# Optimization experiments

Measured on AMD Instinct MI355X. Metric: run time of the kernel, lower is better.

## Reference

```python
import jax, jax.numpy as jnp
import numpy as np

H = 16
D_MODEL = 1024
D_K = D_MODEL // H


def setup_inputs() -> dict:
    key = jax.random.key(0)
    ks = jax.random.split(key, 8)
    B, S = 4, 2048
    query = jax.random.normal(ks[0], (B, S, D_MODEL), dtype=jnp.float32)
    key_t = jax.random.normal(ks[1], (B, S, D_MODEL), dtype=jnp.float32)
    value = jax.random.normal(ks[2], (B, S, D_MODEL), dtype=jnp.float32)
    mask = jax.random.randint(ks[3], (B, S, S), 0, 2, dtype=jnp.int32)
    sc = 1.0 / np.sqrt(D_MODEL)
    Wq = jax.random.normal(ks[4], (D_MODEL, D_MODEL), dtype=jnp.float32) * sc
    Wk = jax.random.normal(ks[5], (D_MODEL, D_MODEL), dtype=jnp.float32) * sc
    Wv = jax.random.normal(ks[6], (D_MODEL, D_MODEL), dtype=jnp.float32) * sc
    Wo = jax.random.normal(ks[7], (D_MODEL, D_MODEL), dtype=jnp.float32) * sc
    return {"query": query, "key": key_t, "value": value, "mask": mask,
            "Wq": Wq, "Wk": Wk, "Wv": Wv, "Wo": Wo}


def reference(query, key, value, mask, Wq, Wk, Wv, Wo):
    B, S, _ = query.shape
    # nn.Linear(bias=False): y = x @ W^T; then split heads -> [B,H,S,d_k]
    def proj(x, W):
        return (x @ W.T).reshape(B, S, H, D_K).transpose(0, 2, 1, 3)

    q = proj(query, Wq)
    k = proj(key, Wk)
    v = proj(value, Wv)

    m = (mask[:, None, :, :] != 0)  # [B,1,S,S] broadcast over heads
    scores = jnp.einsum('bhqd,bhkd->bhqk', q, k) / jnp.sqrt(jnp.float32(D_K))
    scores = jnp.where(m, scores, jnp.float32(-1e9))
    p_attn = jax.nn.softmax(scores, axis=-1)
    p_attn = jnp.where(m, p_attn, 0.0)
    # dropout is identity in eval mode
    x = jnp.einsum('bhqk,bhkd->bhqd', p_attn, v)
    x = x.transpose(0, 2, 1, 3).reshape(B, S, D_MODEL)
    return x @ Wo.T
```

## Files before the change

kernel.cpp:

```cpp
#include <hip/hip_runtime.h>


typedef __attribute__((ext_vector_type(8))) short frag8;
typedef __attribute__((ext_vector_type(4))) float f32x4;
typedef unsigned long long ull;

#define MFMA16(a,b,c) __builtin_amdgcn_mfma_f32_16x16x32_bf16((a),(b),(c),0,0,0)

__device__ __forceinline__ short f2bf(float f) {
  union { float f; unsigned u; } x; x.f = f;
  unsigned r = (x.u + 0x7fffu + ((x.u >> 16) & 1u)) >> 16;
  return (short)r;
}

__device__ __forceinline__ unsigned pkbf(float lo, float hi) {
  union { float f; unsigned u; } a, b;
  a.f = lo; b.f = hi;
  return __builtin_amdgcn_perm(b.u + 0x8000u, a.u + 0x8000u, 0x07060302u);
}

__device__ __forceinline__ unsigned pkbf_t(float lo, float hi) {
  union { float f; unsigned u; } a, b;
  a.f = lo; b.f = hi;
  return __builtin_amdgcn_perm(b.u, a.u, 0x07060302u);
}

__device__ __forceinline__ unsigned bit2m(unsigned word, int off) {
  unsigned r;
  asm("v_bfe_i32 %0, %1, %2, 1" : "=v"(r) : "v"(word), "v"(off));
  return r;
}
__device__ __forceinline__ unsigned mk2(unsigned word, int base) {
  return __builtin_amdgcn_perm(bit2m(word, base + 1), bit2m(word, base),
                               0x05040100u);
}

__device__ __forceinline__ void gl16(const void* g, void* l) {
  __builtin_amdgcn_global_load_lds(
      (const __attribute__((address_space(1))) unsigned*)g,
      (__attribute__((address_space(3))) unsigned*)l, 16, 0, 0);
}

__global__ __launch_bounds__(256) void cast_qkv(
    const float* __restrict__ q, const float* __restrict__ k,
    const float* __restrict__ v, short* __restrict__ qo,
    short* __restrict__ ko, short* __restrict__ vo) {
  int z = blockIdx.x >> 13;
  int i = (blockIdx.x & 8191) * 256 + threadIdx.x;
  const float* s = z == 0 ? q : z == 1 ? k : v;
  short* d = z == 0 ? qo : z == 1 ? ko : vo;
  float4 f = ((const float4*)s)[i];
  short4 o;
  o.x = f2bf(f.x); o.y = f2bf(f.y); o.z = f2bf(f.z); o.w = f2bf(f.w);
  ((short4*)d)[i] = o;
}

__global__ __launch_bounds__(256) void cast_w(
    const float* __restrict__ wq, const float* __restrict__ wk,
    const float* __restrict__ wv, const float* __restrict__ wo,
    short* __restrict__ oq, short* __restrict__ ok,
    short* __restrict__ ov, short* __restrict__ oo) {
  int z = blockIdx.x >> 10;
  int i = (blockIdx.x & 1023) * 256 + threadIdx.x;
  const float* s = z == 0 ? wq : z == 1 ? wk : z == 2 ? wv : wo;
  short* d = z == 0 ? oq : z == 1 ? ok : z == 2 ? ov : oo;
  float sc = (z == 0) ? 0.18033688011f : 1.0f;
  float4 f = ((const float4*)s)[i];
  short4 o;
  o.x = f2bf(f.x * sc); o.y = f2bf(f.y * sc);
  o.z = f2bf(f.z * sc); o.w = f2bf(f.w * sc);
  ((short4*)d)[i] = o;
}

__global__ __launch_bounds__(256) void pack_mask(
    const int* __restrict__ mask, ull* __restrict__ bits) {
  int wv = threadIdx.x >> 6, l = threadIdx.x & 63;
  size_t row = (size_t)blockIdx.x * 4 + wv;
  const int* src = mask + row * 2048;
  for (int c = 0; c < 2048; c += 64) {
    ull bl = __ballot(src[c + l] != 0);
    if (l == 0) bits[(size_t)(c >> 6) * 8192 + row] = bl;
  }
}

template <int MODE>
__device__ __forceinline__ void gemm_body(const short* __restrict__ A,
                                          const short* __restrict__ W,
                                          void* __restrict__ outp, int bid) {
  __shared__ short As[2][128 * 32];
  __shared__ short Bs[2][128 * 32];
  const int t = threadIdx.x;
  const int l = t & 63, wv = t >> 6;
  const int lg = l >> 4, lr = l & 15;
  const int wm = (wv >> 1) * 64, wn = (wv & 1) * 64;
  const int m0 = (bid >> 3) * 128;
  const int n0 = (bid & 7) * 128;

  auto stage = [&](int buf, int kt) {
    const int k0 = kt * 32;
#pragma unroll
    for (int c = 0; c < 2; ++c) {
      int idx = c * 256 + t;
      int row = idx >> 2, ch = (idx & 3) * 8;
      gl16(A + (size_t)(m0 + row) * 1024 + k0 + ch, &As[buf][idx * 8]);
      gl16(W + (size_t)(n0 + row) * 1024 + k0 + ch, &Bs[buf][idx * 8]);
    }
  };

  f32x4 acc[4][4] = {};
  stage(0, 0);
  asm volatile("s_waitcnt vmcnt(0)" ::: "memory");
  __syncthreads();
  int buf = 0;
  for (int kt = 0; kt < 32; ++kt) {
    if (kt + 1 < 32) stage(buf ^ 1, kt + 1);
    frag8 af[4], bf[4];
#pragma unroll
    for (int i = 0; i < 4; ++i) {
      af[i] = *(const frag8*)&As[buf][(wm + i * 16 + lr) * 32 + 8 * lg];
      bf[i] = *(const frag8*)&Bs[buf][(wn + i * 16 + lr) * 32 + 8 * lg];
    }
    __builtin_amdgcn_s_setprio(1);
#pragma unroll
    for (int mi = 0; mi < 4; ++mi)
#pragma unroll
      for (int ni = 0; ni < 4; ++ni)
        acc[mi][ni] = MFMA16(af[mi], bf[ni], acc[mi][ni]);
    __builtin_amdgcn_s_setprio(0);
    asm volatile("s_waitcnt vmcnt(0)" ::: "memory");
    __syncthreads();
    buf ^= 1;
  }

#pragma unroll
  for (int mi = 0; mi < 4; ++mi)
#pragma unroll
    for (int ni = 0; ni < 4; ++ni)
#pragma unroll
      for (int r = 0; r < 4; ++r) {
        int m = m0 + wm + mi * 16 + 4 * lg + r;
        int n = n0 + wn + ni * 16 + lr;
        if (MODE == 0) {
          int b = m >> 11, s = m & 2047, h = n >> 6, dk = n & 63;
          ((short*)outp)[(((size_t)b * 16 + h) * 2048 + s) * 64 + dk] =
              f2bf(acc[mi][ni][r]);
        } else {
          ((float*)outp)[(size_t)m * 1024 + n] = acc[mi][ni][r];
        }
      }
}

__global__ __launch_bounds__(256) void gemm_qkv(
    const short* __restrict__ A0, const short* __restrict__ A1,
    const short* __restrict__ A2, const short* __restrict__ W0,
    const short* __restrict__ W1, const short* __restrict__ W2,
    short* __restrict__ O0, short* __restrict__ O1, short* __restrict__ O2) {
  int wg = (blockIdx.x & 7) * 192 + (blockIdx.x >> 3);
  int z = wg >> 9, bid = wg & 511;
  const short* A = z == 0 ? A0 : z == 1 ? A1 : A2;
  const short* W = z == 0 ? W0 : z == 1 ? W1 : W2;
  short* O = z == 0 ? O0 : z == 1 ? O1 : O2;
  gemm_body<0>(A, W, O, bid);
}

__global__ __launch_bounds__(256) void gemm_o(
    const short* __restrict__ A, const short* __restrict__ W,
    float* __restrict__ O) {
  int bid = (blockIdx.x & 7) * 64 + (blockIdx.x >> 3);
  gemm_body<1>(A, W, O, bid);
}

__global__ __launch_bounds__(256) void transpose_v(
    const short* __restrict__ Vp, short* __restrict__ Vt) {
  __shared__ short lds[64 * 72];
  int bh = blockIdx.y, s0 = blockIdx.x * 64;
  int t = threadIdx.x;
  int rr = t >> 3, c0 = (t & 7) * 8;
#pragma unroll
  for (int half = 0; half < 2; ++half) {
    int r = half * 32 + rr;
    frag8 v = *(const frag8*)(Vp + ((size_t)bh * 2048 + s0 + r) * 64 + c0);
#pragma unroll
    for (int j = 0; j < 8; ++j) lds[r * 72 + c0 + j] = v[j];
  }
  __syncthreads();
#pragma unroll
  for (int half = 0; half < 2; ++half) {
    int d = half * 32 + rr;
    frag8 o;
#pragma unroll
    for (int j = 0; j < 8; ++j) o[j] = lds[(c0 + j) * 72 + d];
    *(frag8*)(Vt + ((size_t)bh * 64 + d) * 2048 + s0 + c0) = o;
  }
}

__global__ __launch_bounds__(256, 4) void attn_fwd(
    const short* __restrict__ Qp, const short* __restrict__ Kp,
    const short* __restrict__ Vt, const ull* __restrict__ mb64,
    short* __restrict__ X) {
  __shared__ short Ks[2][64 * 64];
  __shared__ short Vs[64 * 64];
  __shared__ short Ps[4][16 * 64];

  const int wg = (blockIdx.x & 7) * 128 + (blockIdx.x >> 3);
  const int qt = wg & 15, bh = wg >> 4;
  const int b = bh >> 4, h = bh & 15;
  const int t = threadIdx.x;
  const int l = t & 63, wv = t >> 6;
  const int lg = l >> 4, lr = l & 15;
  const int q0 = qt * 128 + wv * 32;
  const int qrow_base = b << 11;

  frag8 qf[2][2];
  const short* Qb = Qp + ((size_t)bh * 2048 + q0) * 64;
#pragma unroll
  for (int qb = 0; qb < 2; ++qb)
#pragma unroll
    for (int kc = 0; kc < 2; ++kc)
      qf[qb][kc] = *(const frag8*)(Qb + (qb * 16 + lr) * 64 + kc * 32 + 8 * lg);

  f32x4 acc[4][2] = {};
  f32x4 accl[2] = {};

  const size_t kbase = (size_t)bh * 2048 * 64;
  const size_t vbase = (size_t)bh * 64 * 2048;
  short* Pw = &Ps[wv][0];
  const int sx = lr & 7;

  frag8 ones;
#pragma unroll
  for (int j = 0; j < 8; ++j) ones[j] = (short)0x3F80;

  auto stageK = [&](int buf, int kt) {
#pragma unroll
    for (int p = 0; p < 2; ++p) {
      int idx = p * 256 + t;
      int row = idx >> 3, c = idx & 7;
      int cs = (c ^ (row & 7)) * 8;
      gl16(Kp + kbase + (size_t)(kt * 64 + row) * 64 + cs, &Ks[buf][idx * 8]);
    }
  };
  auto stageV = [&](int kt) {
#pragma unroll
    for (int p = 0; p < 2; ++p) {
      int idx = p * 256 + t;
      int row = idx >> 3, c = idx & 7;
      int cs = (c ^ (row & 7)) * 8;
      gl16(Vt + vbase + (size_t)row * 2048 + kt * 64 + cs, &Vs[idx * 8]);
    }
  };

  const uint2* mbp = (const uint2*)mb64;
  const int row0 = qrow_base + q0 + lr;
  const int row1 = row0 + 16;
  uint2 mw0 = mbp[row0], mw1 = mbp[row1];

  stageK(0, 0);
  asm volatile("s_waitcnt vmcnt(0)" ::: "memory");
  __syncthreads();
  int buf = 0;

  for (int kt = 0; kt < 32; ++kt) {
    uint2 mwc0 = mw0, mwc1 = mw1;
    const int nk = (kt + 1) & 31;
    mw0 = mbp[(size_t)nk * 8192 + row0];
    mw1 = mbp[(size_t)nk * 8192 + row1];
    asm volatile("" ::: "memory");
    stageV(kt);
    asm volatile("" ::: "memory");
    stageK(buf ^ 1, nk);

    f32x4 s[4][2] = {};
    __builtin_amdgcn_s_setprio(1);
#pragma unroll
    for (int nb = 0; nb < 4; ++nb) {
      const int ro = (nb * 16 + lr) * 64;
      frag8 k0 = *(const frag8*)&Ks[buf][ro + ((0 + lg) ^ sx) * 8];
      frag8 k1 = *(const frag8*)&Ks[buf][ro + ((4 + lg) ^ sx) * 8];
#pragma unroll
      for (int qb = 0; qb < 2; ++qb) {
        s[nb][qb] = MFMA16(k0, qf[qb][0], s[nb][qb]);
        s[nb][qb] = MFMA16(k1, qf[qb][1], s[nb][qb]);
      }
    }
    __builtin_amdgcn_s_setprio(0);

    auto softmax_store = [&](int qb, uint2 mwq) {
      const int q64 = lr * 64;
#pragma unroll
      for (int nb = 0; nb < 4; ++nb) {
        unsigned word = (nb & 2) ? mwq.y : mwq.x;
        int base = (nb & 1) * 16 + 4 * lg;
        float e0 = __builtin_amdgcn_exp2f(s[nb][qb][0]);
        float e1 = __builtin_amdgcn_exp2f(s[nb][qb][1]);
        float e2 = __builtin_amdgcn_exp2f(s[nb][qb][2]);
        float e3 = __builtin_amdgcn_exp2f(s[nb][qb][3]);
        uint2 w;
        w.x = pkbf_t(e0, e1) & mk2(word, base);
        w.y = pkbf_t(e2, e3) & mk2(word, base + 2);
        int sw = ((2 * nb + (lg >> 1)) ^ sx) * 8 + 4 * (lg & 1);
        *(uint2*)&Pw[q64 + sw] = w;
      }
    };

    softmax_store(0, mwc0);

    asm volatile("s_waitcnt vmcnt(2)" ::: "memory");
    __syncthreads();

    frag8 pf0[2], pf1[2];
#pragma unroll
    for (int kc = 0; kc < 2; ++kc)
      pf0[kc] = *(const frag8*)&Pw[lr * 64 + ((kc * 4 + lg) ^ sx) * 8];
    softmax_store(1, mwc1);
#pragma unroll
    for (int kc = 0; kc < 2; ++kc)
      pf1[kc] = *(const frag8*)&Pw[lr * 64 + ((kc * 4 + lg) ^ sx) * 8];

    __builtin_amdgcn_s_setprio(1);
#pragma unroll
    for (int db = 0; db < 4; ++db) {
      const int ro = (db * 16 + lr) * 64;
      frag8 v0 = *(const frag8*)&Vs[ro + ((0 + lg) ^ sx) * 8];
      frag8 v1 = *(const frag8*)&Vs[ro + ((4 + lg) ^ sx) * 8];
      acc[db][0] = MFMA16(v0, pf0[0], acc[db][0]);
      acc[db][0] = MFMA16(v1, pf0[1], acc[db][0]);
      acc[db][1] = MFMA16(v0, pf1[0], acc[db][1]);
      acc[db][1] = MFMA16(v1, pf1[1], acc[db][1]);
    }
    accl[0] = MFMA16(ones, pf0[0], accl[0]);
    accl[0] = MFMA16(ones, pf0[1], accl[0]);
    accl[1] = MFMA16(ones, pf1[0], accl[1]);
    accl[1] = MFMA16(ones, pf1[1], accl[1]);
    __builtin_amdgcn_s_setprio(0);

    asm volatile("s_waitcnt vmcnt(0)" ::: "memory");
    __syncthreads();
    buf ^= 1;
  }

#pragma unroll
  for (int qb = 0; qb < 2; ++qb) {
    float inv = 1.0f / fmaxf(accl[qb][0], 1e-30f);
    int q = q0 + qb * 16 + lr;
    size_t base = (size_t)(qrow_base + q) * 1024 + h * 64 + 4 * lg;
#pragma unroll
    for (int db = 0; db < 4; ++db) {
      uint2 o;
      o.x = pkbf(acc[db][qb][0] * inv, acc[db][qb][1] * inv);
      o.y = pkbf(acc[db][qb][2] * inv, acc[db][qb][3] * inv);
      *(uint2*)&X[base + db * 16] = o;
    }
  }
}

extern "C" void kernel_launch(void* const* d_in, const int* in_sizes, int n_in,
                              void* d_out, int out_size, void* d_ws,
                              size_t ws_size, hipStream_t stream) {
  const float* q  = (const float*)d_in[0];
  const float* k  = (const float*)d_in[1];
  const float* v  = (const float*)d_in[2];
  const int*  msk = (const int*)d_in[3];
  const float* Wq = (const float*)d_in[4];
  const float* Wk = (const float*)d_in[5];
  const float* Wv = (const float*)d_in[6];
  const float* Wo = (const float*)d_in[7];

  const size_t SZ_T = 16777216;
  const size_t SZ_W = 2097152;
  char* ws = (char*)d_ws;
  short* qb  = (short*)(ws + 0 * SZ_T);
  short* kb  = (short*)(ws + 1 * SZ_T);
  short* vb  = (short*)(ws + 2 * SZ_T);
  short* Qp  = (short*)(ws + 3 * SZ_T);
  short* Kp  = (short*)(ws + 4 * SZ_T);
  short* Vp  = (short*)(ws + 5 * SZ_T);
  short* Vt  = (short*)(ws + 6 * SZ_T);
  short* X   = (short*)(ws + 7 * SZ_T);
  short* wqb = (short*)(ws + 8 * SZ_T);
  short* wkb = (short*)(ws + 8 * SZ_T + 1 * SZ_W);
  short* wvb = (short*)(ws + 8 * SZ_T + 2 * SZ_W);
  short* wob = (short*)(ws + 8 * SZ_T + 3 * SZ_W);
  void*  mb  = (void*)(ws + 8 * SZ_T + 4 * SZ_W);
  if (ws_size < 8 * SZ_T + 5 * SZ_W) return;

  cast_qkv<<<24576, 256, 0, stream>>>(q, k, v, qb, kb, vb);
  cast_w<<<4096, 256, 0, stream>>>(Wq, Wk, Wv, Wo, wqb, wkb, wvb, wob);
  gemm_qkv<<<1536, 256, 0, stream>>>(qb, kb, vb, wqb, wkb, wvb, Qp, Kp, Vp);
  pack_mask<<<2048, 256, 0, stream>>>(msk, (ull*)mb);
  transpose_v<<<dim3(32, 64), 256, 0, stream>>>(Vp, Vt);
  attn_fwd<<<1024, 256, 0, stream>>>(Qp, Kp, Vt, (const ull*)mb, X);
  gemm_o<<<512, 256, 0, stream>>>(X, wob, (float*)d_out);
}
```

Before: 273.8 us.

## Fuse V transpose into QKV GEMM epilogue and delay attention barrier

The V projection now writes its output already transposed. Each wave stages its bf16 tile in LDS inside the GEMM epilogue and stores it to the [b,h,d,s] layout, which removes the separate transpose_v kernel and its extra global read and write of V. In the attention kernel, the barrier and vmcnt wait move after both P-fragment reads, so softmax stores and LDS reads can overlap with outstanding loads. The epilogue relies on per-wave LDS regions starting at As being large enough and not overlapping buffers still in use.

```diff
diff --git a/kernel.cpp b/kernel.cpp
--- a/kernel.cpp
+++ b/kernel.cpp
@@ -132,6 +132,30 @@
     buf ^= 1;
   }
 
+  if (MODE == 2) {
+    short* sl = &As[0][0] + wv * 4096;
+#pragma unroll
+    for (int mi = 0; mi < 4; ++mi)
+#pragma unroll
+      for (int ni = 0; ni < 4; ++ni) {
+        uint2 o;
+        o.x = pkbf(acc[mi][ni][0], acc[mi][ni][1]);
+        o.y = pkbf(acc[mi][ni][2], acc[mi][ni][3]);
+        *(uint2*)&sl[(ni * 16 + lr) * 64 + mi * 16 + 4 * lg] = o;
+      }
+    const int M0 = m0 + wm, N0 = n0 + wn;
+    const int b = M0 >> 11, h = N0 >> 6;
+    short* vt = (short*)outp + (((size_t)b * 16 + h) * 64) * 2048 + (M0 & 2047);
+    asm volatile("s_waitcnt lgkmcnt(0)" ::: "memory");
+#pragma unroll
+    for (int i = 0; i < 16; ++i) {
+      int idx = i * 64 + l;
+      int row = idx >> 4, c4 = (idx & 15) * 4;
+      *(uint2*)&vt[(size_t)row * 2048 + c4] = *(uint2*)&sl[row * 64 + c4];
+    }
+    return;
+  }
+
 #pragma unroll
   for (int mi = 0; mi < 4; ++mi)
 #pragma unroll
@@ -157,10 +181,11 @@
     short* __restrict__ O0, short* __restrict__ O1, short* __restrict__ O2) {
   int wg = (blockIdx.x & 7) * 192 + (blockIdx.x >> 3);
   int z = wg >> 9, bid = wg & 511;
-  const short* A = z == 0 ? A0 : z == 1 ? A1 : A2;
-  const short* W = z == 0 ? W0 : z == 1 ? W1 : W2;
-  short* O = z == 0 ? O0 : z == 1 ? O1 : O2;
-  gemm_body<0>(A, W, O, bid);
+  if (z == 2) {
+    gemm_body<2>(A2, W2, O2, bid);
+  } else {
+    gemm_body<0>(z ? A1 : A0, z ? W1 : W0, z ? O1 : O0, bid);
+  }
 }
 
 __global__ __launch_bounds__(256) void gemm_o(
@@ -168,30 +193,6 @@
     float* __restrict__ O) {
   int bid = (blockIdx.x & 7) * 64 + (blockIdx.x >> 3);
   gemm_body<1>(A, W, O, bid);
-}
-
-__global__ __launch_bounds__(256) void transpose_v(
-    const short* __restrict__ Vp, short* __restrict__ Vt) {
-  __shared__ short lds[64 * 72];
-  int bh = blockIdx.y, s0 = blockIdx.x * 64;
-  int t = threadIdx.x;
-  int rr = t >> 3, c0 = (t & 7) * 8;
-#pragma unroll
-  for (int half = 0; half < 2; ++half) {
-    int r = half * 32 + rr;
-    frag8 v = *(const frag8*)(Vp + ((size_t)bh * 2048 + s0 + r) * 64 + c0);
-#pragma unroll
-    for (int j = 0; j < 8; ++j) lds[r * 72 + c0 + j] = v[j];
-  }
-  __syncthreads();
-#pragma unroll
-  for (int half = 0; half < 2; ++half) {
-    int d = half * 32 + rr;
-    frag8 o;
-#pragma unroll
-    for (int j = 0; j < 8; ++j) o[j] = lds[(c0 + j) * 72 + d];
-    *(frag8*)(Vt + ((size_t)bh * 64 + d) * 2048 + s0 + c0) = o;
-  }
 }
 
 __global__ __launch_bounds__(256, 4) void attn_fwd(
@@ -303,12 +304,8 @@
       }
     };
 
+    frag8 pf0[2], pf1[2];
     softmax_store(0, mwc0);
-
-    asm volatile("s_waitcnt vmcnt(2)" ::: "memory");
-    __syncthreads();
-
-    frag8 pf0[2], pf1[2];
 #pragma unroll
     for (int kc = 0; kc < 2; ++kc)
       pf0[kc] = *(const frag8*)&Pw[lr * 64 + ((kc * 4 + lg) ^ sx) * 8];
@@ -316,6 +313,9 @@
 #pragma unroll
     for (int kc = 0; kc < 2; ++kc)
       pf1[kc] = *(const frag8*)&Pw[lr * 64 + ((kc * 4 + lg) ^ sx) * 8];
+
+    asm volatile("s_waitcnt vmcnt(2)" ::: "memory");
+    __syncthreads();
 
     __builtin_amdgcn_s_setprio(1);
 #pragma unroll
@@ -374,7 +374,6 @@
   short* vb  = (short*)(ws + 2 * SZ_T);
   short* Qp  = (short*)(ws + 3 * SZ_T);
   short* Kp  = (short*)(ws + 4 * SZ_T);
-  short* Vp  = (short*)(ws + 5 * SZ_T);
   short* Vt  = (short*)(ws + 6 * SZ_T);
   short* X   = (short*)(ws + 7 * SZ_T);
   short* wqb = (short*)(ws + 8 * SZ_T);
@@ -386,9 +385,8 @@
 
   cast_qkv<<<24576, 256, 0, stream>>>(q, k, v, qb, kb, vb);
   cast_w<<<4096, 256, 0, stream>>>(Wq, Wk, Wv, Wo, wqb, wkb, wvb, wob);
-  gemm_qkv<<<1536, 256, 0, stream>>>(qb, kb, vb, wqb, wkb, wvb, Qp, Kp, Vp);
+  gemm_qkv<<<1536, 256, 0, stream>>>(qb, kb, vb, wqb, wkb, wvb, Qp, Kp, Vt);
   pack_mask<<<2048, 256, 0, stream>>>(msk, (ull*)mb);
-  transpose_v<<<dim3(32, 64), 256, 0, stream>>>(Vp, Vt);
   attn_fwd<<<1024, 256, 0, stream>>>(Qp, Kp, Vt, (const ull*)mb, X);
   gemm_o<<<512, 256, 0, stream>>>(X, wob, (float*)d_out);
 }
```

Measured after the change: 284.2 us. 3.8% more time.
